# Optimization experiments

Hardware: AMD Instinct MI355X
Metric: run time of the kernel (lower is better)

The kernel has to match this reference:

```python
import jax, jax.numpy as jnp
import numpy as np

B, C, H, W = 4, 32, 540, 960
SY, SX = 2, 2  # upsampling_factor = (2, 2); sH = uf[0], sW = uf[1]; kH = uf[1], kW = uf[0]


def setup_inputs() -> dict:
    key = jax.random.key(0)
    x = jax.random.normal(key, (B, C, H, W), dtype=jnp.float32)
    return {"x": x}


def reference(x) -> jnp.ndarray:
    # ZeroUpsampling: conv_transpose2d with a kernel that is 1 at (0,0) and 0
    # elsewhere, groups=channels, stride=(SY, SX). Mathematically this is a
    # strided scatter: out[..., i*SY, j*SX] = x[..., i, j], zeros elsewhere.
    # Output spatial size matches conv_transpose: (H-1)*SY + kH, kH = SY here.
    b, c, h, w = x.shape
    out_h = (h - 1) * SY + SY  # kernel height == SY for uf=(2,2)
    out_w = (w - 1) * SX + SX
    out = jnp.zeros((b, c, out_h, out_w), dtype=x.dtype)
    return out.at[:, :, ::SY, ::SX].set(x)
```

## Files before the change

kernel.cpp:

```cpp
#include <hip/hip_runtime.h>


constexpr int W_IN  = 960;
constexpr int H_IN  = 540;
constexpr int BC    = 4 * 32;
constexpr int P2PR  = W_IN / 2;
constexpr int OQPR  = (2 * W_IN) / 4;
constexpr long TOTAL = (long)BC * H_IN * P2PR;

__global__ __launch_bounds__(256)
void zero_upsample_kernel(const float2* __restrict__ in2, float4* __restrict__ out) {
    const float4 z = make_float4(0.f, 0.f, 0.f, 0.f);
    const int stride = gridDim.x * blockDim.x;
    for (int t = blockIdx.x * blockDim.x + threadIdx.x; t < (int)TOTAL; t += stride) {
        int r  = t / P2PR;
        int oq = t - r * P2PR;

        float2 v = in2[t];

        int obase = 960 * r + oq;
        out[obase]        = make_float4(v.x, 0.f, v.y, 0.f);
        out[obase + OQPR] = z;
    }
}

extern "C" void kernel_launch(void* const* d_in, const int* in_sizes, int n_in,
                              void* d_out, int out_size, void* d_ws, size_t ws_size,
                              hipStream_t stream) {
    const float2* in2 = (const float2*)d_in[0];
    float4*       out = (float4*)d_out;

    const int block = 256;
    long want = (TOTAL + block - 1) / block;
    int grid = (int)(want < 2048 ? want : 2048);

    zero_upsample_kernel<<<grid, block, 0, stream>>>(in2, out);
}
```

Before: 265.9 us.

## Use 16-byte input loads with per-wave LDS shuffle and nontemporal stores

Each lane now loads a float4 of input instead of a float2, and the values are redistributed within the wave through LDS so each lane writes two contiguous output float4s. The grid is fixed so the stride covers whole input rows, which removes the per-iteration division and leaves only pointer increments. Loads and stores use nontemporal hints to avoid cache pollution on this streaming copy. The cost is an LDS round trip per iteration and hardcoded shapes tied to the exact grid.

```diff
diff --git a/kernel.cpp b/kernel.cpp
--- a/kernel.cpp
+++ b/kernel.cpp
@@ -1,38 +1,73 @@
 #include <hip/hip_runtime.h>
 
+
+typedef float vfloat2 __attribute__((ext_vector_type(2)));
+typedef float vfloat4 __attribute__((ext_vector_type(4)));
 
 constexpr int W_IN  = 960;
 constexpr int H_IN  = 540;
 constexpr int BC    = 4 * 32;
 constexpr int P2PR  = W_IN / 2;
 constexpr int OQPR  = (2 * W_IN) / 4;
-constexpr long TOTAL = (long)BC * H_IN * P2PR;
+constexpr long TOT_F2 = (long)BC * H_IN * P2PR;
+constexpr long TOT_F4 = TOT_F2 / 2;
 
-__global__ __launch_bounds__(256)
-void zero_upsample_kernel(const float2* __restrict__ in2, float4* __restrict__ out) {
-    const float4 z = make_float4(0.f, 0.f, 0.f, 0.f);
-    const int stride = gridDim.x * blockDim.x;
-    for (int t = blockIdx.x * blockDim.x + threadIdx.x; t < (int)TOTAL; t += stride) {
-        int r  = t / P2PR;
-        int oq = t - r * P2PR;
+constexpr int BLOCK = 256;
+constexpr int GRID  = 2025;
+constexpr int WAVES = GRID * (BLOCK / 64);
+constexpr int F4_STRIDE = WAVES * 64;
+constexpr int S2 = F4_STRIDE * 2;
+constexpr int ITERS = (int)(TOT_F4 / F4_STRIDE);
+constexpr int R_STEP = S2 / P2PR;
+constexpr int O_STEP = R_STEP * 2 * OQPR;
 
-        float2 v = in2[t];
+static_assert(S2 % P2PR == 0, "grid stride must be whole input rows");
+static_assert((long)F4_STRIDE * ITERS == TOT_F4, "exact coverage");
 
-        int obase = 960 * r + oq;
-        out[obase]        = make_float4(v.x, 0.f, v.y, 0.f);
-        out[obase + OQPR] = z;
+__global__ __launch_bounds__(BLOCK)
+void zero_upsample_kernel(const vfloat4* __restrict__ in4, vfloat4* __restrict__ out) {
+    __shared__ vfloat4 lds4[BLOCK];
+    const int tid   = blockIdx.x * BLOCK + threadIdx.x;
+    const int wid   = tid >> 6;
+    const int lane  = tid & 63;
+    float* wbuf = (float*)(lds4 + (threadIdx.x & ~63));
+
+    const vfloat4* ip = in4 + tid;
+
+    const int k1 = 128 * wid + lane;
+    const int k2 = k1 + 64;
+    const int r1 = k1 / P2PR, q1 = k1 - P2PR * r1;
+    const int r2 = k2 / P2PR, q2 = k2 - P2PR * r2;
+
+    vfloat4* o1 = out + (size_t)(2 * r1) * OQPR + q1;
+    vfloat4* o2 = out + (size_t)(2 * r2) * OQPR + q2;
+    vfloat4* z1 = o1 + OQPR;
+    vfloat4* z2 = o2 + OQPR;
+
+    const vfloat4 zero = {0.f, 0.f, 0.f, 0.f};
+
+    #pragma unroll 2
+    for (int i = 0; i < ITERS; ++i) {
+        vfloat4 v = __builtin_nontemporal_load(ip);
+        *(vfloat4*)(wbuf + 4 * lane) = v;
+        vfloat2 s1 = *(const vfloat2*)(wbuf + 2 * lane);
+        vfloat2 s2 = *(const vfloat2*)(wbuf + 128 + 2 * lane);
+        vfloat4 e1 = {s1.x, 0.f, s1.y, 0.f};
+        vfloat4 e2 = {s2.x, 0.f, s2.y, 0.f};
+        __builtin_nontemporal_store(e1, o1);
+        __builtin_nontemporal_store(zero, z1);
+        __builtin_nontemporal_store(e2, o2);
+        __builtin_nontemporal_store(zero, z2);
+        ip += F4_STRIDE;
+        o1 += O_STEP;  z1 += O_STEP;
+        o2 += O_STEP;  z2 += O_STEP;
     }
 }
 
 extern "C" void kernel_launch(void* const* d_in, const int* in_sizes, int n_in,
                               void* d_out, int out_size, void* d_ws, size_t ws_size,
                               hipStream_t stream) {
-    const float2* in2 = (const float2*)d_in[0];
-    float4*       out = (float4*)d_out;
-
-    const int block = 256;
-    long want = (TOTAL + block - 1) / block;
-    int grid = (int)(want < 2048 ? want : 2048);
-
-    zero_upsample_kernel<<<grid, block, 0, stream>>>(in2, out);
+    const vfloat4* in4 = (const vfloat4*)d_in[0];
+    vfloat4*       out = (vfloat4*)d_out;
+    zero_upsample_kernel<<<GRID, BLOCK, 0, stream>>>(in4, out);
 }
```

New measurement: 251.8 us. 1.06x faster.
